# Performance work log

Measured on AMD Instinct MI355X. Metric: run time of the kernel, lower is better.

## Reference

```python
import jax, jax.numpy as jnp
import numpy as np

E, S, B, D, F = 8, 2048, 4, 1024, 4096  # experts, seq, batch, d_model, d_ff


def setup_inputs() -> dict:
    key = jax.random.key(0)
    k_x, k_w1, k_w2, k_m = jax.random.split(key, 4)
    scale = 0.02
    x = jax.random.normal(k_x, (S, B, D), dtype=jnp.float32)
    W1 = jax.random.normal(k_w1, (E, D, F), dtype=jnp.float32) * scale
    b1 = jnp.zeros((E, F), dtype=jnp.float32)
    W2 = jax.random.normal(k_w2, (E, F, D), dtype=jnp.float32) * scale
    b2 = jnp.zeros((E, D), dtype=jnp.float32)
    mask = jax.random.randint(k_m, (S, B), 0, E)  # per-token expert id
    return {"x": x, "W1": W1, "b1": b1, "W2": W2, "b2": b2, "mask": mask}


def reference(x, W1, b1, W2, b2, mask):
    # Eval path of ThorFNN: dense all-expert 2-layer FFN, then per-token
    # random expert mask multiply-sum combine. Dropout is identity in eval.
    # h: [E, S, B, F]
    h = jax.nn.relu(jnp.einsum('sbd,edf->esbf', x, W1) + b1[:, None, None, :])
    # out: [E, S, B, D]
    out = jnp.einsum('esbf,efd->esbd', h, W2) + b2[:, None, None, :]
    sel = (mask[None, :, :, None] == jnp.arange(W1.shape[0])[:, None, None, None]).astype(out.dtype)
    return (out * sel).sum(axis=0)  # [S, B, D]
```

## Files before the change

### kernel.cpp

```cpp
#include <hip/hip_runtime.h>
#include <hip/hip_bf16.h>
#include <stdint.h>

#define E_   8
#define S_   2048
#define B_   4
#define D_   1024
#define F_   4096
#define NTOK (S_ * B_)
#define MAXT 72

typedef __attribute__((ext_vector_type(8))) __bf16 bf16x8;
typedef __attribute__((ext_vector_type(4))) float  f32x4;

#define WS_LIST 4096
#define WS_XB   65536
#define WS_W1T  (WS_XB + 16777216)
#define WS_W2T  WS_W1T
#define WS_H    (WS_W1T + 67108864)

__device__ __forceinline__ void gload_lds16(const void* g, void* l) {
    __builtin_amdgcn_global_load_lds(
        (const __attribute__((address_space(1))) void*)g,
        (__attribute__((address_space(3))) void*)l, 16, 0, 0);
}

__global__ void build_lists(const int* __restrict__ mask,
                            int* __restrict__ meta, int* __restrict__ list) {
    __shared__ int cnt[E_], cur[E_];
    int tid = threadIdx.x;
    if (tid < E_) cnt[tid] = 0;
    __syncthreads();
    for (int t = tid; t < NTOK; t += 256) atomicAdd(&cnt[mask[t]], 1);
    __syncthreads();
    if (tid == 0) {
        int acc = 0, nt = 0;
        for (int e = 0; e < E_; ++e) {
            meta[e] = cnt[e];
            meta[8 + e] = acc;
            cur[e] = acc;
            acc += cnt[e];
        }
        for (int e = 0; e < E_; ++e) {
            int mt = (cnt[e] + 127) >> 7;
            for (int m = 0; m < mt; ++m) meta[32 + nt++] = (e << 16) | m;
        }
        meta[16] = nt;
        for (; nt < MAXT; ++nt) meta[32 + nt] = -1;
    }
    __syncthreads();
    for (int t = tid; t < NTOK; t += 256) {
        int e = mask[t];
        int pos = atomicAdd(&cur[e], 1);
        list[pos] = t;
    }
}

__global__ void convert_x_kernel(const float* __restrict__ x,
                                 __hip_bfloat16* __restrict__ xb) {
    size_t i = ((size_t)blockIdx.x * blockDim.x + threadIdx.x) * 4;
    const float4 v = *(const float4*)(x + i);
    union { __hip_bfloat16 h[4]; uint2 u; } o;
    o.h[0] = __float2bfloat16(v.x);
    o.h[1] = __float2bfloat16(v.y);
    o.h[2] = __float2bfloat16(v.z);
    o.h[3] = __float2bfloat16(v.w);
    *(uint2*)(xb + i) = o.u;
}

__global__ void transpose_convert(const float* __restrict__ src,
                                  __hip_bfloat16* __restrict__ dst,
                                  int R, int C) {
    __shared__ float tile[128][33];
    size_t off = (size_t)blockIdx.z * R * C;
    const float* s = src + off;
    __hip_bfloat16* d = dst + off;
    int r0 = blockIdx.y * 128, c0 = blockIdx.x * 32;
    int t = threadIdx.x;
    int rr = t >> 3, cc4 = (t & 7) * 4;
#pragma unroll
    for (int ii = 0; ii < 4; ++ii) {
        float4 v = *(const float4*)(s + (size_t)(r0 + rr + 32 * ii) * C + c0 + cc4);
        tile[rr + 32 * ii][cc4 + 0] = v.x;
        tile[rr + 32 * ii][cc4 + 1] = v.y;
        tile[rr + 32 * ii][cc4 + 2] = v.z;
        tile[rr + 32 * ii][cc4 + 3] = v.w;
    }
    __syncthreads();
    int wc = t >> 5;
    int wr = (t & 31) * 4;
#pragma unroll
    for (int ii = 0; ii < 4; ++ii) {
        int cc = wc + 8 * ii;
        union { __hip_bfloat16 h[4]; uint2 u; } o;
#pragma unroll
        for (int k = 0; k < 4; ++k)
            o.h[k] = __float2bfloat16(tile[wr + k][cc]);
        *(uint2*)(d + (size_t)(c0 + cc) * R + r0 + wr) = o.u;
    }
}

template <int KDIM, int NDIM, int LAYER>
__global__ __launch_bounds__(256, 4) void gemm_kernel(
    const uint8_t* __restrict__ Abase,
    const uint8_t* __restrict__ Wt,
    const float* __restrict__ bias,
    const int* __restrict__ meta, const int* __restrict__ list,
    __hip_bfloat16* __restrict__ Hout, float* __restrict__ Oout) {
    constexpr int NT = NDIM / 128;
    const int nblk = MAXT * NT;
    int orig = blockIdx.x;
    int q = nblk >> 3, r = nblk & 7;
    int xcd = orig & 7, idx = orig >> 3;
    int swz = (xcd < r ? xcd * (q + 1) : r * (q + 1) + (xcd - r) * q) + idx;
    int te = meta[32 + swz / NT];
    if (te < 0) return;
    const int e = te >> 16, mt = te & 0xffff;
    const int cnt = meta[e], bse = meta[8 + e];
    const int n0 = (swz % NT) * 128;
    const int tid = threadIdx.x, wv = tid >> 6, l = tid & 63;
    const int wr = wv >> 1, wc = wv & 1;

    __shared__ __align__(16) uint8_t smem[2][16384];

    const uint8_t* WtE = Wt + (size_t)e * NDIM * KDIM * 2;

    size_t agoff[2], bgoff[2];
#pragma unroll
    for (int p = 0; p < 2; ++p) {
        int rrow = p * 64 + wv * 16 + (l >> 2);
        int grow = mt * 128 + rrow;
        int pidx = bse + (grow < cnt ? grow : cnt - 1);
        size_t arow = (LAYER == 1) ? (size_t)list[pidx] : (size_t)pidx;
        agoff[p] = arow * (KDIM * 2) + (size_t)(l & 3) * 16;
        bgoff[p] = (size_t)(n0 + rrow) * (KDIM * 2) + (size_t)(l & 3) * 16;
    }

    f32x4 acc[4][4] = {};

    auto stage = [&](int buf, int kt) {
        uint8_t* As = &smem[buf][0];
        uint8_t* Bs = &smem[buf][8192];
        size_t kb = (size_t)kt * 64;
#pragma unroll
        for (int p = 0; p < 2; ++p) {
            gload_lds16(Abase + agoff[p] + kb, As + (p * 64 + wv * 16) * 64);
            gload_lds16(WtE + bgoff[p] + kb, Bs + (p * 64 + wv * 16) * 64);
        }
    };

    auto compute = [&](int buf) {
        const uint8_t* As = &smem[buf][0];
        const uint8_t* Bs = &smem[buf][8192];
        bf16x8 a[4], b[4];
#pragma unroll
        for (int mi = 0; mi < 4; ++mi)
            a[mi] = *(const bf16x8*)(As +
                ((wr * 64 + mi * 16 + (l & 15)) * 32 + (l >> 4) * 8) * 2);
#pragma unroll
        for (int ni = 0; ni < 4; ++ni)
            b[ni] = *(const bf16x8*)(Bs +
                ((wc * 64 + ni * 16 + (l & 15)) * 32 + (l >> 4) * 8) * 2);
#pragma unroll
        for (int mi = 0; mi < 4; ++mi)
#pragma unroll
            for (int ni = 0; ni < 4; ++ni)
                acc[mi][ni] = __builtin_amdgcn_mfma_f32_16x16x32_bf16(
                    a[mi], b[ni], acc[mi][ni], 0, 0, 0);
    };

    const int KT = KDIM / 32;
    stage(0, 0);
    __syncthreads();
    int cur = 0;
    for (int kt = 0; kt < KT - 1; ++kt) {
        stage(cur ^ 1, kt + 1);
        compute(cur);
        __syncthreads();
        cur ^= 1;
    }
    compute(cur);

#pragma unroll
    for (int mi = 0; mi < 4; ++mi) {
#pragma unroll
        for (int i = 0; i < 4; ++i) {
            int rl = wr * 64 + mi * 16 + (l >> 4) * 4 + i;
            int grow = mt * 128 + rl;
            if (grow < cnt) {
#pragma unroll
                for (int ni = 0; ni < 4; ++ni) {
                    int col = n0 + wc * 64 + ni * 16 + (l & 15);
                    float v = acc[mi][ni][i] + bias[(size_t)e * NDIM + col];
                    if (LAYER == 1) {
                        v = fmaxf(v, 0.f);
                        Hout[(size_t)(bse + grow) * NDIM + col] = __float2bfloat16(v);
                    } else {
                        int tok = list[bse + grow];
                        Oout[(size_t)tok * NDIM + col] = v;
                    }
                }
            }
        }
    }
}

extern "C" void kernel_launch(void* const* d_in, const int* in_sizes, int n_in,
                              void* d_out, int out_size, void* d_ws, size_t ws_size,
                              hipStream_t stream) {
    const float* x  = (const float*)d_in[0];
    const float* W1 = (const float*)d_in[1];
    const float* b1 = (const float*)d_in[2];
    const float* W2 = (const float*)d_in[3];
    const float* b2 = (const float*)d_in[4];
    const int* mask = (const int*)d_in[5];
    float* out = (float*)d_out;

    uint8_t* ws = (uint8_t*)d_ws;
    int* meta = (int*)ws;
    int* list = (int*)(ws + WS_LIST);
    __hip_bfloat16* xb  = (__hip_bfloat16*)(ws + WS_XB);
    __hip_bfloat16* w1t = (__hip_bfloat16*)(ws + WS_W1T);
    __hip_bfloat16* w2t = (__hip_bfloat16*)(ws + WS_W2T);
    __hip_bfloat16* H   = (__hip_bfloat16*)(ws + WS_H);

    build_lists<<<1, 256, 0, stream>>>(mask, meta, list);
    convert_x_kernel<<<NTOK * D_ / 4 / 256, 256, 0, stream>>>(x, xb);
    transpose_convert<<<dim3(F_ / 32, D_ / 128, E_), 256, 0, stream>>>(W1, w1t, D_, F_);
    gemm_kernel<D_, F_, 1><<<MAXT * (F_ / 128), 256, 0, stream>>>(
        (const uint8_t*)xb, (const uint8_t*)w1t, b1, meta, list, H, nullptr);
    transpose_convert<<<dim3(D_ / 32, F_ / 128, E_), 256, 0, stream>>>(W2, w2t, F_, D_);
    gemm_kernel<F_, D_, 2><<<MAXT * (D_ / 128), 256, 0, stream>>>(
        (const uint8_t*)H, (const uint8_t*)w2t, b2, meta, list, nullptr, out);
}
```

Before: 568.0 us.

## Swizzle GEMM LDS layout and transpose weights in registers with wide stores

Replaces the shared-memory tiled weight transpose with a register-based 8x8 per-thread transpose over 128x128 tiles, emitting 16-byte bf16 stores. Applies an XOR swizzle to the 16-byte chunk position in LDS for both A and B tiles, consistently on the async global-to-LDS load side and the fragment read side, to reduce bank conflicts in MFMA operand loads. The register transpose uses more registers per thread, and its strided global reads may coalesce less well.

After: 568.7 us. No clear change (+0.1%).

```diff
diff --git a/kernel.cpp b/kernel.cpp
--- a/kernel.cpp
+++ b/kernel.cpp
@@ -71,32 +71,26 @@
 __global__ void transpose_convert(const float* __restrict__ src,
                                   __hip_bfloat16* __restrict__ dst,
                                   int R, int C) {
-    __shared__ float tile[128][33];
     size_t off = (size_t)blockIdx.z * R * C;
     const float* s = src + off;
     __hip_bfloat16* d = dst + off;
-    int r0 = blockIdx.y * 128, c0 = blockIdx.x * 32;
+    int r0 = blockIdx.y * 128, c0 = blockIdx.x * 128;
     int t = threadIdx.x;
-    int rr = t >> 3, cc4 = (t & 7) * 4;
-#pragma unroll
-    for (int ii = 0; ii < 4; ++ii) {
-        float4 v = *(const float4*)(s + (size_t)(r0 + rr + 32 * ii) * C + c0 + cc4);
-        tile[rr + 32 * ii][cc4 + 0] = v.x;
-        tile[rr + 32 * ii][cc4 + 1] = v.y;
-        tile[rr + 32 * ii][cc4 + 2] = v.z;
-        tile[rr + 32 * ii][cc4 + 3] = v.w;
-    }
-    __syncthreads();
-    int wc = t >> 5;
-    int wr = (t & 31) * 4;
-#pragma unroll
-    for (int ii = 0; ii < 4; ++ii) {
-        int cc = wc + 8 * ii;
-        union { __hip_bfloat16 h[4]; uint2 u; } o;
-#pragma unroll
-        for (int k = 0; k < 4; ++k)
-            o.h[k] = __float2bfloat16(tile[wr + k][cc]);
-        *(uint2*)(d + (size_t)(c0 + cc) * R + r0 + wr) = o.u;
+    int rb = t >> 4, cb = t & 15;
+    const float* sp = s + (size_t)(r0 + 8 * rb) * C + c0 + 8 * cb;
+    float v[8][8];
+#pragma unroll
+    for (int j = 0; j < 8; ++j) {
+        *(float4*)&v[j][0] = *(const float4*)(sp + (size_t)j * C);
+        *(float4*)&v[j][4] = *(const float4*)(sp + (size_t)j * C + 4);
+    }
+    __hip_bfloat16* dp = d + (size_t)(c0 + 8 * cb) * R + r0 + 8 * rb;
+#pragma unroll
+    for (int i = 0; i < 8; ++i) {
+        union { __hip_bfloat16 h[8]; uint4 u; } o;
+#pragma unroll
+        for (int j = 0; j < 8; ++j) o.h[j] = __float2bfloat16(v[j][i]);
+        *(uint4*)(dp + (size_t)i * R) = o.u;
     }
 }
 
@@ -132,8 +126,9 @@
         int grow = mt * 128 + rrow;
         int pidx = bse + (grow < cnt ? grow : cnt - 1);
         size_t arow = (LAYER == 1) ? (size_t)list[pidx] : (size_t)pidx;
-        agoff[p] = arow * (KDIM * 2) + (size_t)(l & 3) * 16;
-        bgoff[p] = (size_t)(n0 + rrow) * (KDIM * 2) + (size_t)(l & 3) * 16;
+        size_t chunk = (size_t)(((l & 3) ^ ((l >> 3) & 3)) * 16);
+        agoff[p] = arow * (KDIM * 2) + chunk;
+        bgoff[p] = (size_t)(n0 + rrow) * (KDIM * 2) + chunk;
     }
 
     f32x4 acc[4][4] = {};
@@ -154,13 +149,17 @@
         const uint8_t* Bs = &smem[buf][8192];
         bf16x8 a[4], b[4];
 #pragma unroll
-        for (int mi = 0; mi < 4; ++mi)
-            a[mi] = *(const bf16x8*)(As +
-                ((wr * 64 + mi * 16 + (l & 15)) * 32 + (l >> 4) * 8) * 2);
-#pragma unroll
-        for (int ni = 0; ni < 4; ++ni)
-            b[ni] = *(const bf16x8*)(Bs +
-                ((wc * 64 + ni * 16 + (l & 15)) * 32 + (l >> 4) * 8) * 2);
+        for (int mi = 0; mi < 4; ++mi) {
+            int row = wr * 64 + mi * 16 + (l & 15);
+            a[mi] = *(const bf16x8*)(As + row * 64 +
+                                     (((l >> 4) ^ ((row >> 1) & 3)) << 4));
+        }
+#pragma unroll
+        for (int ni = 0; ni < 4; ++ni) {
+            int row = wc * 64 + ni * 16 + (l & 15);
+            b[ni] = *(const bf16x8*)(Bs + row * 64 +
+                                     (((l >> 4) ^ ((row >> 1) & 3)) << 4));
+        }
 #pragma unroll
         for (int mi = 0; mi < 4; ++mi)
 #pragma unroll
@@ -226,10 +225,10 @@
 
     build_lists<<<1, 256, 0, stream>>>(mask, meta, list);
     convert_x_kernel<<<NTOK * D_ / 4 / 256, 256, 0, stream>>>(x, xb);
-    transpose_convert<<<dim3(F_ / 32, D_ / 128, E_), 256, 0, stream>>>(W1, w1t, D_, F_);
+    transpose_convert<<<dim3(F_ / 128, D_ / 128, E_), 256, 0, stream>>>(W1, w1t, D_, F_);
     gemm_kernel<D_, F_, 1><<<MAXT * (F_ / 128), 256, 0, stream>>>(
         (const uint8_t*)xb, (const uint8_t*)w1t, b1, meta, list, H, nullptr);
-    transpose_convert<<<dim3(D_ / 32, F_ / 128, E_), 256, 0, stream>>>(W2, w2t, F_, D_);
+    transpose_convert<<<dim3(D_ / 128, F_ / 128, E_), 256, 0, stream>>>(W2, w2t, F_, D_);
     gemm_kernel<F_, D_, 2><<<MAXT * (D_ / 128), 256, 0, stream>>>(
         (const uint8_t*)H, (const uint8_t*)w2t, b2, meta, list, nullptr, out);
 }
```
